# Optimization experiments

Measured on AMD Instinct MI355X. Metric: run time of the kernel, lower is better.

Reference implementation:

```python
import jax, jax.numpy as jnp
import numpy as np

NU, NT, NV = 20000, 50000, 100000   # user / travel / visit_area node counts
DU, DT = 64, 32                      # raw user / travel feature dims
H, L, E = 128, 8, 500000             # hidden, num_layers, edges per edge type
EPS = 1e-5


def _ln(x, g, b):
    m = x.mean(-1, keepdims=True)
    v = ((x - m) ** 2).mean(-1, keepdims=True)
    return (x - m) * jax.lax.rsqrt(v + EPS) * g + b


def _sage(x_src, x_dst, ei, Wl, bl, Wr, n_dst):
    # PyG SAGEConv: mean-aggregate source features over incoming edges,
    # transform with lin_l (bias), plus root transform lin_r (no bias).
    msg = jax.ops.segment_sum(x_src[ei[0]], ei[1], num_segments=n_dst)
    cnt = jax.ops.segment_sum(jnp.ones((ei.shape[1],), x_src.dtype), ei[1], num_segments=n_dst)
    mean = msg / jnp.maximum(cnt, 1.0)[:, None]
    return mean @ Wl + bl + x_dst @ Wr


def setup_inputs() -> dict:
    key = jax.random.key(0)
    ks = iter(jax.random.split(key, 64))
    f = lambda shape, s: jax.random.normal(next(ks), shape, jnp.float32) * s
    ei = lambda ns, nd: jnp.stack([
        jax.random.randint(next(ks), (E,), 0, ns, dtype=jnp.int32),
        jax.random.randint(next(ks), (E,), 0, nd, dtype=jnp.int32)])
    return {
        "x_user": jax.random.normal(next(ks), (NU, DU), jnp.float32),
        "x_travel": jax.random.normal(next(ks), (NT, DT), jnp.float32),
        "x_visit": jax.random.normal(next(ks), (NV, H), jnp.float32),
        "W_in_user": f((DU, H), 0.1), "b_in_user": jnp.zeros((H,), jnp.float32),
        "W_in_travel": f((DT, H), 0.1), "b_in_travel": jnp.zeros((H,), jnp.float32),
        # edge-type order: 0=user->travel, 1=travel->user, 2=travel->visit, 3=visit->travel
        "Wl": f((L, 4, H, H), 0.05), "bl": jnp.zeros((L, 4, H), jnp.float32),
        "Wr": f((L, 4, H, H), 0.05),
        # node-type order for norms: 0=user, 1=travel, 2=visit_area
        "ln_g": jnp.ones((L, 3, H), jnp.float32), "ln_b": jnp.zeros((L, 3, H), jnp.float32),
        # 3 expert MLPs (location / preference / category)
        "e_ln_g": jnp.ones((3, H), jnp.float32), "e_ln_b": jnp.zeros((3, H), jnp.float32),
        "e_W1": f((3, H, H), 0.05), "e_b1": jnp.zeros((3, H), jnp.float32),
        "e_W2": f((3, H, H // 2), 0.05), "e_b2": jnp.zeros((3, H // 2), jnp.float32),
        "e_W3": f((3, H // 2, 1), 0.05), "e_b3": jnp.zeros((3, 1), jnp.float32),
        # MultiheadAttention gate (4 heads) + learned query
        "attn_query": f((H,), 1.0),
        "Wq": f((H, H), 0.05), "bq": jnp.zeros((H,), jnp.float32),
        "Wk": f((H, H), 0.05), "bk": jnp.zeros((H,), jnp.float32),
        "Wv": f((H, H), 0.05), "bv": jnp.zeros((H,), jnp.float32),
        "Wo": f((H, H), 0.05), "bo": jnp.zeros((H,), jnp.float32),
        "f_ln_g": jnp.ones((H,), jnp.float32), "f_ln_b": jnp.zeros((H,), jnp.float32),
        "f_W1": f((H, H), 0.05), "f_b1": jnp.zeros((H,), jnp.float32),
        "f_W2": f((H, 1), 0.05), "f_b2": jnp.zeros((1,), jnp.float32),
        "ei_ut": ei(NU, NT), "ei_tu": ei(NT, NU),
        "ei_tv": ei(NT, NV), "ei_vt": ei(NV, NT),
    }


def reference(x_user, x_travel, x_visit,
              W_in_user, b_in_user, W_in_travel, b_in_travel,
              Wl, bl, Wr, ln_g, ln_b,
              e_ln_g, e_ln_b, e_W1, e_b1, e_W2, e_b2, e_W3, e_b3,
              attn_query, Wq, bq, Wk, bk, Wv, bv, Wo, bo,
              f_ln_g, f_ln_b, f_W1, f_b1, f_W2, f_b2,
              ei_ut, ei_tu, ei_tv, ei_vt):
    xu = x_user @ W_in_user + b_in_user
    xt = x_travel @ W_in_travel + b_in_travel
    xv = x_visit  # Identity projection
    for i in range(L):
        hu = _sage(xt, xu, ei_tu, Wl[i, 1], bl[i, 1], Wr[i, 1], NU)
        ht = (_sage(xu, xt, ei_ut, Wl[i, 0], bl[i, 0], Wr[i, 0], NT)
              + _sage(xv, xt, ei_vt, Wl[i, 3], bl[i, 3], Wr[i, 3], NT))  # HeteroConv aggr='sum'
        hv = _sage(xt, xv, ei_tv, Wl[i, 2], bl[i, 2], Wr[i, 2], NV)
        # dropout is identity in eval mode
        xu = jax.nn.relu(_ln(hu, ln_g[i, 0], ln_b[i, 0])) + xu
        xt = jax.nn.relu(_ln(ht, ln_g[i, 1], ln_b[i, 1])) + xt
        xv = jax.nn.relu(_ln(hv, ln_g[i, 2], ln_b[i, 2])) + xv
    h = xv  # [NV, H]
    # expert heads are computed in the torch forward but do NOT feed final_score
    _experts = [
        jax.nn.relu(jax.nn.relu(_ln(h, e_ln_g[j], e_ln_b[j]) @ e_W1[j] + e_b1[j])
                    @ e_W2[j] + e_b2[j]) @ e_W3[j] + e_b3[j]
        for j in range(3)
    ]
    # attention gate: 1 query token vs 1 key/value token per node -> softmax over 1 key == 1
    nh, hd = 4, H // 4
    Q = (attn_query @ Wq + bq).reshape(nh, hd)        # shared query
    Kh = (h @ Wk + bk).reshape(-1, nh, hd)
    Vh = (h @ Wv + bv).reshape(-1, nh, hd)
    s = (Q[None] * Kh).sum(-1) / jnp.sqrt(jnp.float32(hd))   # [NV, nh]
    w = jax.nn.softmax(s[..., None], axis=-1)                 # exactly ones
    attn = (w * Vh).reshape(-1, H) @ Wo + bo
    z = jax.nn.relu(_ln(attn, f_ln_g, f_ln_b) @ f_W1 + f_b1)  # final dropout = identity (eval)
    return (z @ f_W2 + f_b2)[:, 0]
```

## Files before the change

kernel.cpp:

```cpp
#include <hip/hip_runtime.h>

typedef float v4f __attribute__((ext_vector_type(4)));
typedef _Float16 h4 __attribute__((ext_vector_type(4)));
typedef _Float16 h8 __attribute__((ext_vector_type(8)));

namespace {

constexpr int NU = 20000;
constexpr int NT = 50000;
constexpr int NV = 100000;
constexpr int HD = 128;
constexpr int LAYERS = 8;
constexpr float EPS = 1e-5f;

constexpr int NUP = 20032, NTP = 50048, NVP = 100032;

constexpr int AGS = 136;
constexpr int HBS = 132;
constexpr int SCB = 2048;

__device__ __forceinline__ float wave_sum(float v) {
#pragma unroll
    for (int m = 32; m >= 1; m >>= 1) v += __shfl_xor(v, m, 64);
    return v;
}
__device__ __forceinline__ int wave_sum_i(int v) {
#pragma unroll
    for (int m = 32; m >= 1; m >>= 1) v += __shfl_xor(v, m, 64);
    return v;
}
__device__ __forceinline__ float qsum16(float v) {
#pragma unroll
    for (int m = 8; m >= 1; m >>= 1) v += __shfl_xor(v, m, 64);
    return v;
}


struct CsrJob {
    const int* src; const int* dst;
    int* cur; int* rp; int* col; float* inv;
    int n;
};
struct CsrJobs { CsrJob j[4]; };

__global__ void hist_all_kernel(CsrJobs J, int E, int nbPer) {
    const int which = blockIdx.x / nbPer;
    const int e = (blockIdx.x - which * nbPer) * 256 + threadIdx.x;
    if (e < E) atomicAdd(&J.j[which].cur[J.j[which].dst[e]], 1);
}

__global__ __launch_bounds__(256) void csr_psum_kernel(CsrJobs J, int* __restrict__ part) {
    const int which = blockIdx.x >> 6;
    const int b = blockIdx.x & 63;
    const CsrJob& job = J.j[which];
    const int n = job.n;
    const int base = b * SCB;
    __shared__ int ws[4];
    int s = 0;
    if (base < n) {
        const int end = min(base + SCB, n);
        for (int i = base + threadIdx.x; i < end; i += 256) s += job.cur[i];
    }
    int sw = wave_sum_i(s);
    if ((threadIdx.x & 63) == 0) ws[threadIdx.x >> 6] = sw;
    __syncthreads();
    if (threadIdx.x == 0) part[which * 64 + b] = ws[0] + ws[1] + ws[2] + ws[3];
}

__global__ __launch_bounds__(64) void csr_pscan_kernel(int* __restrict__ part) {
    const int which = blockIdx.x;
    const int t = threadIdx.x;
    int v = part[which * 64 + t];
#pragma unroll
    for (int off = 1; off < 64; off <<= 1) {
        int u = __shfl_up(v, off, 64);
        if (t >= off) v += u;
    }
    int ex = __shfl_up(v, 1, 64);
    if (t == 0) ex = 0;
    part[which * 64 + t] = ex;
}

__global__ __launch_bounds__(256) void csr_scan_kernel(CsrJobs J, const int* __restrict__ part) {
    const int which = blockIdx.x >> 6;
    const int b = blockIdx.x & 63;
    const CsrJob& job = J.j[which];
    const int n = job.n;
    const int base = b * SCB;
    if (base >= n) return;
    const int t = threadIdx.x;
    __shared__ int tsum[256];
    int d[8];
    const int i0 = base + t * 8;
    int s = 0;
#pragma unroll
    for (int k = 0; k < 8; ++k) {
        const int i = i0 + k;
        d[k] = (i < n) ? job.cur[i] : 0;
        s += d[k];
    }
    tsum[t] = s;
    __syncthreads();
    for (int off = 1; off < 256; off <<= 1) {
        int u = (t >= off) ? tsum[t - off] : 0;
        __syncthreads();
        tsum[t] += u;
        __syncthreads();
    }
    int run = part[which * 64 + b] + ((t == 0) ? 0 : tsum[t - 1]);
#pragma unroll
    for (int k = 0; k < 8; ++k) {
        const int i = i0 + k;
        if (i < n) {
            job.rp[i] = run;
            job.inv[i] = 1.0f / (float)max(d[k], 1);
            job.cur[i] = run;
            run += d[k];
            if (i == n - 1) job.rp[n] = run;
        }
    }
}

__global__ void scatter_all_kernel(CsrJobs J, int E, int nbPer) {
    const int which = blockIdx.x / nbPer;
    const int e = (blockIdx.x - which * nbPer) * 256 + threadIdx.x;
    if (e < E) {
        const CsrJob& job = J.j[which];
        int p = atomicAdd(&job.cur[job.dst[e]], 1);
        job.col[p] = job.src[e];
    }
}


__global__ __launch_bounds__(256) void tw_kernel(const float* __restrict__ Wl,
                                                 const float* __restrict__ Wr,
                                                 _Float16* __restrict__ WT) {
    const int slot = blockIdx.x;
    const int layer = slot / 7, j = slot % 7;
    const float* A;
    const float* B = nullptr;
    if (j < 4) A = Wl + ((size_t)layer * 4 + j) * 16384;
    else if (j == 4) {
        A = Wr + ((size_t)layer * 4 + 0) * 16384;
        B = Wr + ((size_t)layer * 4 + 3) * 16384;
    } else A = Wr + ((size_t)layer * 4 + (j - 4)) * 16384;
    _Float16* o = WT + (size_t)slot * 16384;
    for (int idx = threadIdx.x; idx < 16384; idx += 256) {
        const int n = idx >> 7, k = idx & 127;
        float v = A[k * 128 + n];
        if (j == 4) v += B[k * 128 + n];
        o[idx] = (_Float16)v;
    }
}


__global__ __launch_bounds__(256) void cast_kernel(const float* __restrict__ X,
                                                   _Float16* __restrict__ Y, int n4) {
    int i = blockIdx.x * 256 + threadIdx.x;
    if (i < n4) {
        v4f x = *(const v4f*)(X + (size_t)i * 4);
        h4 y;
        y[0] = (_Float16)x.x; y[1] = (_Float16)x.y;
        y[2] = (_Float16)x.z; y[3] = (_Float16)x.w;
        *(h4*)(Y + (size_t)i * 4) = y;
    }
}


#define ACC_H8(vh, X, Y)                                                         \
    {                                                                            \
        X.x += (float)vh[0]; X.y += (float)vh[1];                                \
        X.z += (float)vh[2]; X.w += (float)vh[3];                                \
        Y.x += (float)vh[4]; Y.y += (float)vh[5];                                \
        Y.z += (float)vh[6]; Y.w += (float)vh[7];                                \
    }

__device__ __forceinline__ void gather_row_h(
    const _Float16* __restrict__ src, const int* __restrict__ colg,
    const int* __restrict__ sCol, int off_r, int s0, int e1,
    int c8, float iv, _Float16* __restrict__ outRow, int cap) {
    const int d = e1 - s0;
    const int jst = min(d, max(0, cap - off_r));
    v4f aA = {0.f, 0.f, 0.f, 0.f}, aB = aA, bA = aA, bB = aA;
    int j = 0;
    for (; j + 8 <= jst; j += 8) {
        h8 v0 = *(const h8*)(src + (size_t)sCol[off_r + j + 0] * 128 + c8);
        h8 v1 = *(const h8*)(src + (size_t)sCol[off_r + j + 1] * 128 + c8);
        h8 v2 = *(const h8*)(src + (size_t)sCol[off_r + j + 2] * 128 + c8);
        h8 v3 = *(const h8*)(src + (size_t)sCol[off_r + j + 3] * 128 + c8);
        h8 v4 = *(const h8*)(src + (size_t)sCol[off_r + j + 4] * 128 + c8);
        h8 v5 = *(const h8*)(src + (size_t)sCol[off_r + j + 5] * 128 + c8);
        h8 v6 = *(const h8*)(src + (size_t)sCol[off_r + j + 6] * 128 + c8);
        h8 v7 = *(const h8*)(src + (size_t)sCol[off_r + j + 7] * 128 + c8);
        ACC_H8(v0, aA, aB); ACC_H8(v1, bA, bB);
        ACC_H8(v2, aA, aB); ACC_H8(v3, bA, bB);
        ACC_H8(v4, aA, aB); ACC_H8(v5, bA, bB);
        ACC_H8(v6, aA, aB); ACC_H8(v7, bA, bB);
    }
    for (; j < jst; ++j) {
        h8 v0 = *(const h8*)(src + (size_t)sCol[off_r + j] * 128 + c8);
        ACC_H8(v0, aA, aB);
    }
    for (int e = s0 + jst; e < e1; ++e) {
        h8 v0 = *(const h8*)(src + (size_t)colg[e] * 128 + c8);
        ACC_H8(v0, aA, aB);
    }
    v4f r0 = (aA + bA) * iv;
    v4f r1 = (aB + bB) * iv;
    h8 o;
    o[0] = (_Float16)r0.x; o[1] = (_Float16)r0.y; o[2] = (_Float16)r0.z; o[3] = (_Float16)r0.w;
    o[4] = (_Float16)r1.x; o[5] = (_Float16)r1.y; o[6] = (_Float16)r1.z; o[7] = (_Float16)r1.w;
    *(h8*)(outRow + c8) = o;
}


template <int HAS2>
__device__ __forceinline__ void sage_mfma_body(
    int row0, int nrows,
    const float* __restrict__ xdst, float* __restrict__ out,
    _Float16* __restrict__ out_h, const _Float16* __restrict__ xdh,
    const _Float16* __restrict__ src1h, const int* __restrict__ rp1,
    const int* __restrict__ col1, const float* __restrict__ inv1,
    const _Float16* __restrict__ Wl1T, const float* __restrict__ bl1,
    const _Float16* __restrict__ src2h, const int* __restrict__ rp2,
    const int* __restrict__ col2, const float* __restrict__ inv2,
    const _Float16* __restrict__ Wl2T, const float* __restrict__ bl2,
    const _Float16* __restrict__ WrTh,
    const float* __restrict__ g, const float* __restrict__ bln,
    _Float16* aggH1, _Float16* aggH2, float* hbuf, int* sC1, int* sC2, int cap) {
    const int t = threadIdx.x;
    const int w = t >> 6, l = t & 63;
    const int m = l & 15, q = l >> 4;
    const int c8 = m * 8;
    const int rows_end = min(row0 + 64, nrows);

    const int eb1 = rp1[row0];
    const int cnt1 = min(rp1[rows_end] - eb1, cap);
    for (int i = t; i < cnt1; i += 256) sC1[i] = col1[eb1 + i];
    int eb2 = 0;
    if constexpr (HAS2) {
        eb2 = rp2[row0];
        const int cnt2 = min(rp2[rows_end] - eb2, cap);
        for (int i = t; i < cnt2; i += 256) sC2[i] = col2[eb2 + i];
    }
    __syncthreads();

#pragma unroll
    for (int i = 0; i < 4; ++i) {
        const int rloc = w * 16 + q * 4 + i;
        const int gr = row0 + rloc;
        if (gr < nrows) {
            {
                const int s0 = rp1[gr], e1r = rp1[gr + 1];
                gather_row_h(src1h, col1, sC1, s0 - eb1, s0, e1r, c8, inv1[gr],
                             aggH1 + (size_t)rloc * AGS, cap);
            }
            if constexpr (HAS2) {
                const int s0 = rp2[gr], e1r = rp2[gr + 1];
                gather_row_h(src2h, col2, sC2, s0 - eb2, s0, e1r, c8, inv2[gr],
                             aggH2 + (size_t)rloc * AGS, cap);
            }
        }
    }

    v4f acc[8];
#pragma unroll
    for (int nt = 0; nt < 8; ++nt) acc[nt] = (v4f){0.f, 0.f, 0.f, 0.f};

    const _Float16* xdrow = xdh + (size_t)(row0 + w * 16 + m) * 128;
#pragma unroll
    for (int kt = 0; kt < 4; ++kt) {
        h8 a = *(const h8*)(xdrow + kt * 32 + q * 8);
#pragma unroll
        for (int nt = 0; nt < 8; ++nt) {
            h8 b = *(const h8*)(WrTh + (size_t)(nt * 16 + m) * 128 + kt * 32 + q * 8);
            acc[nt] = __builtin_amdgcn_mfma_f32_16x16x32_f16(a, b, acc[nt], 0, 0, 0);
        }
    }
    __syncthreads();

    const _Float16* arow1 = aggH1 + (size_t)(w * 16 + m) * AGS;
#pragma unroll
    for (int kt = 0; kt < 4; ++kt) {
        h8 a = *(const h8*)(arow1 + kt * 32 + q * 8);
#pragma unroll
        for (int nt = 0; nt < 8; ++nt) {
            h8 b = *(const h8*)(Wl1T + (size_t)(nt * 16 + m) * 128 + kt * 32 + q * 8);
            acc[nt] = __builtin_amdgcn_mfma_f32_16x16x32_f16(a, b, acc[nt], 0, 0, 0);
        }
    }
    if constexpr (HAS2) {
        const _Float16* arow2 = aggH2 + (size_t)(w * 16 + m) * AGS;
#pragma unroll
        for (int kt = 0; kt < 4; ++kt) {
            h8 a = *(const h8*)(arow2 + kt * 32 + q * 8);
#pragma unroll
            for (int nt = 0; nt < 8; ++nt) {
                h8 b = *(const h8*)(Wl2T + (size_t)(nt * 16 + m) * 128 + kt * 32 + q * 8);
                acc[nt] = __builtin_amdgcn_mfma_f32_16x16x32_f16(a, b, acc[nt], 0, 0, 0);
            }
        }
    }
    __syncthreads();

#pragma unroll
    for (int nt = 0; nt < 8; ++nt)
#pragma unroll
        for (int r = 0; r < 4; ++r)
            hbuf[(size_t)(w * 16 + q * 4 + r) * HBS + nt * 16 + m] = acc[nt][r];
    __syncthreads();

    v4f bg0 = *(const v4f*)&bl1[c8];
    v4f bg1 = *(const v4f*)&bl1[c8 + 4];
    if constexpr (HAS2) {
        bg0 += *(const v4f*)&bl2[c8];
        bg1 += *(const v4f*)&bl2[c8 + 4];
    }
    v4f g0 = *(const v4f*)&g[c8], g1 = *(const v4f*)&g[c8 + 4];
    v4f lb0 = *(const v4f*)&bln[c8], lb1 = *(const v4f*)&bln[c8 + 4];
#pragma unroll
    for (int i = 0; i < 4; ++i) {
        const int rloc = w * 16 + q * 4 + i;
        const int gr = row0 + rloc;
        if (gr >= nrows) continue;
        v4f h0 = *(const v4f*)&hbuf[(size_t)rloc * HBS + c8] + bg0;
        v4f h1 = *(const v4f*)&hbuf[(size_t)rloc * HBS + c8 + 4] + bg1;
        float part = h0.x + h0.y + h0.z + h0.w + h1.x + h1.y + h1.z + h1.w;
        float mean = qsum16(part) * (1.0f / 128.0f);
        v4f d0 = h0 - mean, d1 = h1 - mean;
        float vp = d0.x * d0.x + d0.y * d0.y + d0.z * d0.z + d0.w * d0.w +
                   d1.x * d1.x + d1.y * d1.y + d1.z * d1.z + d1.w * d1.w;
        float var = qsum16(vp) * (1.0f / 128.0f);
        float rs = rsqrtf(var + EPS);
        v4f x0 = *(const v4f*)&xdst[(size_t)gr * 128 + c8];
        v4f x1 = *(const v4f*)&xdst[(size_t)gr * 128 + c8 + 4];
        v4f y0, y1;
#pragma unroll
        for (int e = 0; e < 4; ++e) {
            y0[e] = fmaxf(d0[e] * rs * g0[e] + lb0[e], 0.f) + x0[e];
            y1[e] = fmaxf(d1[e] * rs * g1[e] + lb1[e], 0.f) + x1[e];
        }
        *(v4f*)&out[(size_t)gr * 128 + c8] = y0;
        *(v4f*)&out[(size_t)gr * 128 + c8 + 4] = y1;
        h8 oh;
#pragma unroll
        for (int e = 0; e < 4; ++e) {
            oh[e] = (_Float16)y0[e];
            oh[4 + e] = (_Float16)y1[e];
        }
        *(h8*)&out_h[(size_t)gr * 128 + c8] = oh;
    }
}

__global__ __launch_bounds__(256, 3) void travel_mfma(
    const float* xdst, float* out, _Float16* out_h, const _Float16* xdh,
    const _Float16* src1h, const int* rp1, const int* col1, const float* inv1,
    const _Float16* Wl1T, const float* bl1,
    const _Float16* src2h, const int* rp2, const int* col2, const float* inv2,
    const _Float16* Wl2T, const float* bl2,
    const _Float16* WrTh, const float* g, const float* bln) {
    __shared__ __align__(16) char smem[34816 + 8192];
    _Float16* aggH1 = (_Float16*)smem;
    _Float16* aggH2 = (_Float16*)(smem + 17408);
    float* hbuf = (float*)smem;
    int* sC1 = (int*)(smem + 34816);
    int* sC2 = sC1 + 1024;
    sage_mfma_body<1>(blockIdx.x * 64, NT, xdst, out, out_h, xdh,
                      src1h, rp1, col1, inv1, Wl1T, bl1,
                      src2h, rp2, col2, inv2, Wl2T, bl2,
                      WrTh, g, bln, aggH1, aggH2, hbuf, sC1, sC2, 1024);
}

struct UpdParams {
    const float* xdst; float* out; _Float16* out_h;
    const _Float16* srch; const int* rp; const int* col; const float* inv;
    const _Float16* WlT; const float* bl; const _Float16* WrT;
    const float* g; const float* bln;
    int nrows;
};

__global__ __launch_bounds__(256, 3) void uv_mfma(UpdParams U, UpdParams V, int nbU) {
    __shared__ __align__(16) char smem[33792 + 8192];
    _Float16* aggH1 = (_Float16*)smem;
    float* hbuf = (float*)smem;
    int* sC1 = (int*)(smem + 33792);
    const bool isU = (int)blockIdx.x < nbU;
    const UpdParams& P = isU ? U : V;
    const int row0 = (isU ? blockIdx.x : blockIdx.x - nbU) * 64;
    sage_mfma_body<0>(row0, P.nrows, P.xdst, P.out, P.out_h, P.out_h,
                      P.srch, P.rp, P.col, P.inv, P.WlT, P.bl,
                      nullptr, nullptr, nullptr, nullptr, nullptr, nullptr,
                      P.WrT, P.g, P.bln, aggH1, nullptr, hbuf, sC1, nullptr, 2048);
}


template <int K, bool LN_IN, bool RELU, bool MIRROR>
__global__ __launch_bounds__(256) void gemm_kernel(const float* __restrict__ X,
                                                   const float* __restrict__ W,
                                                   const float* __restrict__ bias,
                                                   float* __restrict__ Y,
                                                   _Float16* __restrict__ Yh,
                                                   const float* __restrict__ g,
                                                   const float* __restrict__ bln) {
    static_assert(!LN_IN || K == 128, "LN input requires K==128");
    __shared__ __align__(16) float As[16 * K];
    const int t = threadIdx.x;
    const size_t row0 = (size_t)blockIdx.x * 16;

    for (int idx = t; idx < 16 * K; idx += 256) As[idx] = X[row0 * K + idx];
    __syncthreads();

    if (LN_IN) {
        const int w = t >> 6, l = t & 63;
        for (int qq = 0; qq < 4; ++qq) {
            const int r = w * 4 + qq;
            float a0 = As[r * K + l], a1 = As[r * K + 64 + l];
            float mm = wave_sum(a0 + a1) * (1.0f / 128.0f);
            float d0 = a0 - mm, d1 = a1 - mm;
            float var = wave_sum(d0 * d0 + d1 * d1) * (1.0f / 128.0f);
            float rs = rsqrtf(var + EPS);
            As[r * K + l] = d0 * rs * g[l] + bln[l];
            As[r * K + 64 + l] = d1 * rs * g[64 + l] + bln[64 + l];
        }
        __syncthreads();
    }

    const int c0 = (t & 31) * 4;
    const int r0 = (t >> 5) * 2;
    v4f b4 = *(const v4f*)&bias[c0];
    v4f acc0 = b4, acc1 = b4;
#pragma unroll 4
    for (int k = 0; k < K; k += 4) {
        v4f a0 = *(const v4f*)&As[r0 * K + k];
        v4f a1 = *(const v4f*)&As[(r0 + 1) * K + k];
        v4f w0 = *(const v4f*)&W[(size_t)(k + 0) * HD + c0];
        v4f w1 = *(const v4f*)&W[(size_t)(k + 1) * HD + c0];
        v4f w2 = *(const v4f*)&W[(size_t)(k + 2) * HD + c0];
        v4f w3 = *(const v4f*)&W[(size_t)(k + 3) * HD + c0];
        acc0 += a0.x * w0 + a0.y * w1 + a0.z * w2 + a0.w * w3;
        acc1 += a1.x * w0 + a1.y * w1 + a1.z * w2 + a1.w * w3;
    }
    if (RELU) {
#pragma unroll
        for (int i = 0; i < 4; ++i) {
            acc0[i] = fmaxf(acc0[i], 0.0f);
            acc1[i] = fmaxf(acc1[i], 0.0f);
        }
    }
    *(v4f*)&Y[(row0 + r0) * HD + c0] = acc0;
    *(v4f*)&Y[(row0 + r0 + 1) * HD + c0] = acc1;
    if (MIRROR) {
        h4 m0, m1;
#pragma unroll
        for (int i = 0; i < 4; ++i) {
            m0[i] = (_Float16)acc0[i];
            m1[i] = (_Float16)acc1[i];
        }
        *(h4*)&Yh[(row0 + r0) * HD + c0] = m0;
        *(h4*)&Yh[(row0 + r0 + 1) * HD + c0] = m1;
    }
}


__global__ __launch_bounds__(128) void fold_kernel(const float* __restrict__ Wv,
                                                   const float* __restrict__ bv,
                                                   const float* __restrict__ Wo,
                                                   const float* __restrict__ bo,
                                                   float* __restrict__ Wvo,
                                                   float* __restrict__ bvo) {
    const int c = threadIdx.x;
    const int r = blockIdx.x;
    if (r < 128) {
        float s = 0.f;
        for (int k = 0; k < 128; ++k) s += Wv[r * 128 + k] * Wo[k * 128 + c];
        Wvo[r * 128 + c] = s;
    } else {
        float s = bo[c];
        for (int k = 0; k < 128; ++k) s += bv[k] * Wo[k * 128 + c];
        bvo[c] = s;
    }
}


__global__ __launch_bounds__(256) void dot_kernel(const float* __restrict__ Z,
                                                  const float* __restrict__ w2,
                                                  const float* __restrict__ b2,
                                                  float* __restrict__ out, int n) {
    const int w = threadIdx.x >> 6, l = threadIdx.x & 63;
    const size_t row = (size_t)blockIdx.x * 4 + w;
    if (row < (size_t)n) {
        float v = Z[row * 128 + l] * w2[l] + Z[row * 128 + 64 + l] * w2[64 + l];
        v = wave_sum(v);
        if (l == 0) out[row] = v + b2[0];
    }
}

}

extern "C" void kernel_launch(void* const* d_in, const int* in_sizes, int n_in,
                              void* d_out, int out_size, void* d_ws, size_t ws_size,
                              hipStream_t stream) {
    const float* x_user     = (const float*)d_in[0];
    const float* x_travel   = (const float*)d_in[1];
    float*       xv         = (float*)d_in[2];
    const float* W_in_user  = (const float*)d_in[3];
    const float* b_in_user  = (const float*)d_in[4];
    const float* W_in_travel= (const float*)d_in[5];
    const float* b_in_travel= (const float*)d_in[6];
    const float* Wl         = (const float*)d_in[7];
    const float* bl         = (const float*)d_in[8];
    const float* Wr         = (const float*)d_in[9];
    const float* ln_g       = (const float*)d_in[10];
    const float* ln_b       = (const float*)d_in[11];
    const float* Wv_        = (const float*)d_in[25];
    const float* bv_        = (const float*)d_in[26];
    const float* Wo_        = (const float*)d_in[27];
    const float* bo_        = (const float*)d_in[28];
    const float* f_ln_g     = (const float*)d_in[29];
    const float* f_ln_b     = (const float*)d_in[30];
    const float* f_W1       = (const float*)d_in[31];
    const float* f_b1       = (const float*)d_in[32];
    const float* f_W2       = (const float*)d_in[33];
    const float* f_b2       = (const float*)d_in[34];
    const int*   ei_ut      = (const int*)d_in[35];
    const int*   ei_tu      = (const int*)d_in[36];
    const int*   ei_tv      = (const int*)d_in[37];
    const int*   ei_vt      = (const int*)d_in[38];
    const int E = in_sizes[35] / 2;

    char* wsb = (char*)d_ws;
    size_t off = 0;
    auto alloc = [&](size_t bytes) -> void* {
        off = (off + 511) & ~(size_t)511;
        void* p = wsb + off;
        off += bytes;
        return p;
    };
    float* xu = (float*)alloc((size_t)NU * HD * 4);
    float* xt = (float*)alloc((size_t)NT * HD * 4);
    _Float16* xu_h  = (_Float16*)alloc((size_t)NUP * HD * 2);
    _Float16* xv_h  = (_Float16*)alloc((size_t)NVP * HD * 2);
    _Float16* xt_h0 = (_Float16*)alloc((size_t)NTP * HD * 2);
    _Float16* xt_h1 = (_Float16*)alloc((size_t)NTP * HD * 2);
    _Float16* WT = (_Float16*)alloc((size_t)LAYERS * 7 * 16384 * 2);
    float* Wvo = (float*)alloc(128 * 128 * 4);
    float* bvo = (float*)alloc(128 * 4);
    int* part = (int*)alloc(4 * 64 * 4);

    const int ndst[4] = {NU, NT, NT, NV};
    int* cur4 = (int*)alloc((size_t)(NU + NT + NT + NV) * 4);
    int *rp[4], *colb[4];
    float* invb[4];
    int* cur[4];
    {
        int coff = 0;
        for (int i = 0; i < 4; ++i) {
            cur[i] = cur4 + coff;
            coff += ndst[i];
            rp[i]   = (int*)alloc((size_t)(ndst[i] + 1) * 4);
            colb[i] = (int*)alloc((size_t)E * 4);
            invb[i] = (float*)alloc((size_t)ndst[i] * 4);
        }
    }

    hipMemsetAsync(cur4, 0, (size_t)(NU + NT + NT + NV) * 4, stream);
    CsrJobs J;
    J.j[0] = { ei_tu, ei_tu + E, cur[0], rp[0], colb[0], invb[0], NU };
    J.j[1] = { ei_ut, ei_ut + E, cur[1], rp[1], colb[1], invb[1], NT };
    J.j[2] = { ei_vt, ei_vt + E, cur[2], rp[2], colb[2], invb[2], NT };
    J.j[3] = { ei_tv, ei_tv + E, cur[3], rp[3], colb[3], invb[3], NV };
    const int nbPer = (E + 255) / 256;
    hist_all_kernel<<<4 * nbPer, 256, 0, stream>>>(J, E, nbPer);
    csr_psum_kernel<<<4 * 64, 256, 0, stream>>>(J, part);
    csr_pscan_kernel<<<4, 64, 0, stream>>>(part);
    csr_scan_kernel<<<4 * 64, 256, 0, stream>>>(J, part);
    scatter_all_kernel<<<4 * nbPer, 256, 0, stream>>>(J, E, nbPer);

    tw_kernel<<<LAYERS * 7, 256, 0, stream>>>(Wl, Wr, WT);

    gemm_kernel<64, false, false, true><<<NU / 16, 256, 0, stream>>>(
        x_user, W_in_user, b_in_user, xu, xu_h, nullptr, nullptr);
    gemm_kernel<32, false, false, true><<<NT / 16, 256, 0, stream>>>(
        x_travel, W_in_travel, b_in_travel, xt, xt_h0, nullptr, nullptr);
    cast_kernel<<<(NV * HD / 4 + 255) / 256, 256, 0, stream>>>(xv, xv_h, NV * HD / 4);

    const int nbU = (NU + 63) / 64;
    const int nbV = (NV + 63) / 64;
    const int nbT = (NT + 63) / 64;
    for (int i = 0; i < LAYERS; ++i) {
        const _Float16* WTl = WT + (size_t)i * 7 * 16384;
        const float* bl_i = bl + (size_t)i * 4 * 128;
        const float* g_i  = ln_g + (size_t)i * 3 * 128;
        const float* b_i  = ln_b + (size_t)i * 3 * 128;
        _Float16* xth_cur = (i & 1) ? xt_h1 : xt_h0;
        _Float16* xth_nxt = (i & 1) ? xt_h0 : xt_h1;
        travel_mfma<<<nbT, 256, 0, stream>>>(
            xt, xt, xth_nxt, xth_cur,
            xu_h, rp[1], colb[1], invb[1], WTl + 0 * 16384, bl_i + 0 * 128,
            xv_h, rp[2], colb[2], invb[2], WTl + 3 * 16384, bl_i + 3 * 128,
            WTl + 4 * 16384, g_i + 1 * 128, b_i + 1 * 128);
        UpdParams U = { xu, xu, xu_h, xth_cur, rp[0], colb[0], invb[0],
                        WTl + 1 * 16384, bl_i + 1 * 128, WTl + 5 * 16384,
                        g_i + 0 * 128, b_i + 0 * 128, NU };
        UpdParams V = { xv, xv, xv_h, xth_cur, rp[3], colb[3], invb[3],
                        WTl + 2 * 16384, bl_i + 2 * 128, WTl + 6 * 16384,
                        g_i + 2 * 128, b_i + 2 * 128, NV };
        uv_mfma<<<nbU + nbV, 256, 0, stream>>>(U, V, nbU);
    }

    fold_kernel<<<129, 128, 0, stream>>>(Wv_, bv_, Wo_, bo_, Wvo, bvo);
    float* attn = (float*)xu_h;
    gemm_kernel<128, false, false, false><<<NV / 16, 256, 0, stream>>>(
        xv, Wvo, bvo, attn, nullptr, nullptr, nullptr);
    gemm_kernel<128, true, true, false><<<NV / 16, 256, 0, stream>>>(
        attn, f_W1, f_b1, attn, nullptr, f_ln_g, f_ln_b);
    dot_kernel<<<NV / 4, 256, 0, stream>>>(attn, f_W2, f_b2, (float*)d_out, NV);
}
```

Before: 2.441 ms.

## Fuse per-layer travel and user/visit updates into one launch; partition CSR atomics by range

Double-buffers the fp16 user and visit feature copies so the travel update and the user/visit updates of a layer can run concurrently in a single fused kernel launch, removing one launch and its dependency barrier per layer. The fused path is enabled only when the workspace is large enough, otherwise it falls back to two launches. The CSR histogram and scatter kernels now process edge chunks per block and split destinations into 8 ranges, so each block's atomics hit a narrower address range, at the cost of reading each edge index 8 times. The fused launch also raises shared-memory usage for update blocks to the travel size.

After: 2.166 ms. 1.13x faster.

```diff
diff --git a/kernel.cpp b/kernel.cpp
--- a/kernel.cpp
+++ b/kernel.cpp
@@ -18,6 +18,7 @@
 constexpr int AGS = 136;
 constexpr int HBS = 132;
 constexpr int SCB = 2048;
+constexpr int ECH = 2048;
 
 __device__ __forceinline__ float wave_sum(float v) {
 #pragma unroll
@@ -43,10 +44,22 @@
 };
 struct CsrJobs { CsrJob j[4]; };
 
-__global__ void hist_all_kernel(CsrJobs J, int E, int nbPer) {
-    const int which = blockIdx.x / nbPer;
-    const int e = (blockIdx.x - which * nbPer) * 256 + threadIdx.x;
-    if (e < E) atomicAdd(&J.j[which].cur[J.j[which].dst[e]], 1);
+
+__global__ __launch_bounds__(256) void hist_all_kernel(CsrJobs J, int E, int nbPer) {
+    const int r = blockIdx.x & 7;
+    const int rest = blockIdx.x >> 3;
+    const int which = rest / nbPer;
+    const int chunk = rest - which * nbPer;
+    const CsrJob& job = J.j[which];
+    const int n = job.n;
+    const int lo = r * (n >> 3);
+    const int hi = (r == 7) ? n : lo + (n >> 3);
+    const int base = chunk * ECH;
+    const int end = min(base + ECH, E);
+    for (int e = base + threadIdx.x; e < end; e += 256) {
+        const int d = job.dst[e];
+        if (d >= lo && d < hi) atomicAdd(&job.cur[d], 1);
+    }
 }
 
 __global__ __launch_bounds__(256) void csr_psum_kernel(CsrJobs J, int* __restrict__ part) {
@@ -121,13 +134,23 @@
     }
 }
 
-__global__ void scatter_all_kernel(CsrJobs J, int E, int nbPer) {
-    const int which = blockIdx.x / nbPer;
-    const int e = (blockIdx.x - which * nbPer) * 256 + threadIdx.x;
-    if (e < E) {
-        const CsrJob& job = J.j[which];
-        int p = atomicAdd(&job.cur[job.dst[e]], 1);
-        job.col[p] = job.src[e];
+__global__ __launch_bounds__(256) void scatter_all_kernel(CsrJobs J, int E, int nbPer) {
+    const int r = blockIdx.x & 7;
+    const int rest = blockIdx.x >> 3;
+    const int which = rest / nbPer;
+    const int chunk = rest - which * nbPer;
+    const CsrJob& job = J.j[which];
+    const int n = job.n;
+    const int lo = r * (n >> 3);
+    const int hi = (r == 7) ? n : lo + (n >> 3);
+    const int base = chunk * ECH;
+    const int end = min(base + ECH, E);
+    for (int e = base + threadIdx.x; e < end; e += 256) {
+        const int d = job.dst[e];
+        if (d >= lo && d < hi) {
+            int p = atomicAdd(&job.cur[d], 1);
+            job.col[p] = job.src[e];
+        }
     }
 }
 
@@ -352,45 +375,50 @@
     }
 }
 
-__global__ __launch_bounds__(256, 3) void travel_mfma(
-    const float* xdst, float* out, _Float16* out_h, const _Float16* xdh,
-    const _Float16* src1h, const int* rp1, const int* col1, const float* inv1,
-    const _Float16* Wl1T, const float* bl1,
-    const _Float16* src2h, const int* rp2, const int* col2, const float* inv2,
-    const _Float16* Wl2T, const float* bl2,
-    const _Float16* WrTh, const float* g, const float* bln) {
-    __shared__ __align__(16) char smem[34816 + 8192];
-    _Float16* aggH1 = (_Float16*)smem;
-    _Float16* aggH2 = (_Float16*)(smem + 17408);
-    float* hbuf = (float*)smem;
-    int* sC1 = (int*)(smem + 34816);
-    int* sC2 = sC1 + 1024;
-    sage_mfma_body<1>(blockIdx.x * 64, NT, xdst, out, out_h, xdh,
-                      src1h, rp1, col1, inv1, Wl1T, bl1,
-                      src2h, rp2, col2, inv2, Wl2T, bl2,
-                      WrTh, g, bln, aggH1, aggH2, hbuf, sC1, sC2, 1024);
-}
+struct TrvParams {
+    const float* xdst; float* out; _Float16* out_h; const _Float16* xdh;
+    const _Float16* src1h; const int* rp1; const int* col1; const float* inv1;
+    const _Float16* Wl1T; const float* bl1;
+    const _Float16* src2h; const int* rp2; const int* col2; const float* inv2;
+    const _Float16* Wl2T; const float* bl2;
+    const _Float16* WrTh; const float* g; const float* bln;
+};
 
 struct UpdParams {
-    const float* xdst; float* out; _Float16* out_h;
+    const float* xdst; float* out; _Float16* out_h; const _Float16* xdh;
     const _Float16* srch; const int* rp; const int* col; const float* inv;
     const _Float16* WlT; const float* bl; const _Float16* WrT;
     const float* g; const float* bln;
     int nrows;
 };
 
-__global__ __launch_bounds__(256, 3) void uv_mfma(UpdParams U, UpdParams V, int nbU) {
-    __shared__ __align__(16) char smem[33792 + 8192];
-    _Float16* aggH1 = (_Float16*)smem;
-    float* hbuf = (float*)smem;
-    int* sC1 = (int*)(smem + 33792);
-    const bool isU = (int)blockIdx.x < nbU;
-    const UpdParams& P = isU ? U : V;
-    const int row0 = (isU ? blockIdx.x : blockIdx.x - nbU) * 64;
-    sage_mfma_body<0>(row0, P.nrows, P.xdst, P.out, P.out_h, P.out_h,
-                      P.srch, P.rp, P.col, P.inv, P.WlT, P.bl,
-                      nullptr, nullptr, nullptr, nullptr, nullptr, nullptr,
-                      P.WrT, P.g, P.bln, aggH1, nullptr, hbuf, sC1, nullptr, 2048);
+__global__ __launch_bounds__(256, 3) void layer_mfma(TrvParams T, UpdParams U, UpdParams V,
+                                                     int nbT, int nbU) {
+    __shared__ __align__(16) char smem[34816 + 8192];
+    int b = blockIdx.x;
+    if (b < nbT) {
+        _Float16* aggH1 = (_Float16*)smem;
+        _Float16* aggH2 = (_Float16*)(smem + 17408);
+        float* hbuf = (float*)smem;
+        int* sC1 = (int*)(smem + 34816);
+        int* sC2 = sC1 + 1024;
+        sage_mfma_body<1>(b * 64, NT, T.xdst, T.out, T.out_h, T.xdh,
+                          T.src1h, T.rp1, T.col1, T.inv1, T.Wl1T, T.bl1,
+                          T.src2h, T.rp2, T.col2, T.inv2, T.Wl2T, T.bl2,
+                          T.WrTh, T.g, T.bln, aggH1, aggH2, hbuf, sC1, sC2, 1024);
+    } else {
+        b -= nbT;
+        const bool isU = b < nbU;
+        const UpdParams& P = isU ? U : V;
+        const int row0 = (isU ? b : b - nbU) * 64;
+        _Float16* aggH1 = (_Float16*)smem;
+        float* hbuf = (float*)smem;
+        int* sC1 = (int*)(smem + 34816);
+        sage_mfma_body<0>(row0, P.nrows, P.xdst, P.out, P.out_h, P.xdh,
+                          P.srch, P.rp, P.col, P.inv, P.WlT, P.bl,
+                          nullptr, nullptr, nullptr, nullptr, nullptr, nullptr,
+                          P.WrT, P.g, P.bln, aggH1, nullptr, hbuf, sC1, nullptr, 2048);
+    }
 }
 
 
@@ -528,6 +556,9 @@
     const int*   ei_vt      = (const int*)d_in[38];
     const int E = in_sizes[35] / 2;
 
+    constexpr size_t FUSED_NEED = (size_t)140 << 20;
+    const bool fused = ws_size >= FUSED_NEED;
+
     char* wsb = (char*)d_ws;
     size_t off = 0;
     auto alloc = [&](size_t bytes) -> void* {
@@ -538,10 +569,20 @@
     };
     float* xu = (float*)alloc((size_t)NU * HD * 4);
     float* xt = (float*)alloc((size_t)NT * HD * 4);
-    _Float16* xu_h  = (_Float16*)alloc((size_t)NUP * HD * 2);
-    _Float16* xv_h  = (_Float16*)alloc((size_t)NVP * HD * 2);
-    _Float16* xt_h0 = (_Float16*)alloc((size_t)NTP * HD * 2);
-    _Float16* xt_h1 = (_Float16*)alloc((size_t)NTP * HD * 2);
+    _Float16* xu_h[2];
+    _Float16* xv_h[2];
+    _Float16* xt_h[2];
+    xu_h[0] = (_Float16*)alloc((size_t)NUP * HD * 2);
+    xv_h[0] = (_Float16*)alloc((size_t)NVP * HD * 2);
+    xt_h[0] = (_Float16*)alloc((size_t)NTP * HD * 2);
+    xt_h[1] = (_Float16*)alloc((size_t)NTP * HD * 2);
+    if (fused) {
+        xu_h[1] = (_Float16*)alloc((size_t)NUP * HD * 2);
+        xv_h[1] = (_Float16*)alloc((size_t)NVP * HD * 2);
+    } else {
+        xu_h[1] = xu_h[0];
+        xv_h[1] = xv_h[0];
+    }
     _Float16* WT = (_Float16*)alloc((size_t)LAYERS * 7 * 16384 * 2);
     float* Wvo = (float*)alloc(128 * 128 * 4);
     float* bvo = (float*)alloc(128 * 4);
@@ -569,20 +610,20 @@
     J.j[1] = { ei_ut, ei_ut + E, cur[1], rp[1], colb[1], invb[1], NT };
     J.j[2] = { ei_vt, ei_vt + E, cur[2], rp[2], colb[2], invb[2], NT };
     J.j[3] = { ei_tv, ei_tv + E, cur[3], rp[3], colb[3], invb[3], NV };
-    const int nbPer = (E + 255) / 256;
-    hist_all_kernel<<<4 * nbPer, 256, 0, stream>>>(J, E, nbPer);
+    const int nbPerC = (E + ECH - 1) / ECH;
+    hist_all_kernel<<<4 * nbPerC * 8, 256, 0, stream>>>(J, E, nbPerC);
     csr_psum_kernel<<<4 * 64, 256, 0, stream>>>(J, part);
     csr_pscan_kernel<<<4, 64, 0, stream>>>(part);
     csr_scan_kernel<<<4 * 64, 256, 0, stream>>>(J, part);
-    scatter_all_kernel<<<4 * nbPer, 256, 0, stream>>>(J, E, nbPer);
+    scatter_all_kernel<<<4 * nbPerC * 8, 256, 0, stream>>>(J, E, nbPerC);
 
     tw_kernel<<<LAYERS * 7, 256, 0, stream>>>(Wl, Wr, WT);
 
     gemm_kernel<64, false, false, true><<<NU / 16, 256, 0, stream>>>(
-        x_user, W_in_user, b_in_user, xu, xu_h, nullptr, nullptr);
+        x_user, W_in_user, b_in_user, xu, xu_h[0], nullptr, nullptr);
     gemm_kernel<32, false, false, true><<<NT / 16, 256, 0, stream>>>(
-        x_travel, W_in_travel, b_in_travel, xt, xt_h0, nullptr, nullptr);
-    cast_kernel<<<(NV * HD / 4 + 255) / 256, 256, 0, stream>>>(xv, xv_h, NV * HD / 4);
+        x_travel, W_in_travel, b_in_travel, xt, xt_h[0], nullptr, nullptr);
+    cast_kernel<<<(NV * HD / 4 + 255) / 256, 256, 0, stream>>>(xv, xv_h[0], NV * HD / 4);
 
     const int nbU = (NU + 63) / 64;
     const int nbV = (NV + 63) / 64;
@@ -592,24 +633,27 @@
         const float* bl_i = bl + (size_t)i * 4 * 128;
         const float* g_i  = ln_g + (size_t)i * 3 * 128;
         const float* b_i  = ln_b + (size_t)i * 3 * 128;
-        _Float16* xth_cur = (i & 1) ? xt_h1 : xt_h0;
-        _Float16* xth_nxt = (i & 1) ? xt_h0 : xt_h1;
-        travel_mfma<<<nbT, 256, 0, stream>>>(
-            xt, xt, xth_nxt, xth_cur,
-            xu_h, rp[1], colb[1], invb[1], WTl + 0 * 16384, bl_i + 0 * 128,
-            xv_h, rp[2], colb[2], invb[2], WTl + 3 * 16384, bl_i + 3 * 128,
-            WTl + 4 * 16384, g_i + 1 * 128, b_i + 1 * 128);
-        UpdParams U = { xu, xu, xu_h, xth_cur, rp[0], colb[0], invb[0],
+        const int c = i & 1, nx = c ^ 1;
+        TrvParams T = { xt, xt, xt_h[nx], xt_h[c],
+                        xu_h[c], rp[1], colb[1], invb[1], WTl + 0 * 16384, bl_i + 0 * 128,
+                        xv_h[c], rp[2], colb[2], invb[2], WTl + 3 * 16384, bl_i + 3 * 128,
+                        WTl + 4 * 16384, g_i + 1 * 128, b_i + 1 * 128 };
+        UpdParams U = { xu, xu, xu_h[nx], xu_h[c], xt_h[c], rp[0], colb[0], invb[0],
                         WTl + 1 * 16384, bl_i + 1 * 128, WTl + 5 * 16384,
                         g_i + 0 * 128, b_i + 0 * 128, NU };
-        UpdParams V = { xv, xv, xv_h, xth_cur, rp[3], colb[3], invb[3],
+        UpdParams V = { xv, xv, xv_h[nx], xv_h[c], xt_h[c], rp[3], colb[3], invb[3],
                         WTl + 2 * 16384, bl_i + 2 * 128, WTl + 6 * 16384,
                         g_i + 2 * 128, b_i + 2 * 128, NV };
-        uv_mfma<<<nbU + nbV, 256, 0, stream>>>(U, V, nbU);
+        if (fused) {
+            layer_mfma<<<nbT + nbU + nbV, 256, 0, stream>>>(T, U, V, nbT, nbU);
+        } else {
+            layer_mfma<<<nbT, 256, 0, stream>>>(T, U, V, nbT, nbU);
+            layer_mfma<<<nbU + nbV, 256, 0, stream>>>(T, U, V, 0, nbU);
+        }
     }
 
     fold_kernel<<<129, 128, 0, stream>>>(Wv_, bv_, Wo_, bo_, Wvo, bvo);
-    float* attn = (float*)xu_h;
+    float* attn = (float*)xu_h[0];
     gemm_kernel<128, false, false, false><<<NV / 16, 256, 0, stream>>>(
         xv, Wvo, bvo, attn, nullptr, nullptr, nullptr);
     gemm_kernel<128, true, true, false><<<NV / 16, 256, 0, stream>>>(
```
